# Kernel tuning notes

Hardware: AMD Instinct MI355X
Metric: run time of the kernel (lower is better)

Reference implementation:

```python
import jax, jax.numpy as jnp
import numpy as np

N = 256
DIAM = 2.0 * np.pi
VISC = 1e-3
DRAG = 0.1
SCALE = 1.0
PEAK_K = 4
DT = 0.001            # stable_time_step: min(0.001, 0.5*dx/max_velocity) = 0.001 here
NUM_STEPS = 90        # int(T/0.001), T=0.09
RECORD_EVERY = 30
BATCH = 8

# Carpenter-Kennedy low-storage RK4 / Crank-Nicolson tableau (jax-cfd crank_nicolson_rk4)
ALPHAS = (0.0, 0.1496590219993, 0.3704009573644, 0.6222557631345, 0.9582821306748, 1.0)
BETAS = (0.0, -0.4178904745, -1.192151694643, -1.697784692471, -1.514183444257)
GAMMAS = (0.1496590219993, 0.3792103129999, 0.8229550293869, 0.6994504559488, 0.1530572479681)


def _consts():
    kx = jnp.fft.fftfreq(N, d=DIAM / N).astype(jnp.float32)      # cycles / unit length
    ky = jnp.fft.rfftfreq(N, d=DIAM / N).astype(jnp.float32)
    KX, KY = jnp.meshgrid(kx, ky, indexing='ij')                 # [N, N//2+1]
    lap = -(2.0 * np.pi) ** 2 * (KX ** 2 + KY ** 2)              # (2*pi*i*k)^2, real
    lap_nz = lap.at[0, 0].set(1.0)
    # 2/3-rule brick wall dealiasing filter
    third = N // 3
    filt = jnp.zeros((N, N // 2 + 1), jnp.float32)
    filt = filt.at[:third, :third + 1].set(1.0)
    filt = filt.at[-third:, :third + 1].set(1.0)
    # Kolmogorov forcing u=(scale*sin(k y), 0) -> vorticity forcing -scale*k*cos(k y)
    y = (jnp.arange(N, dtype=jnp.float32) + 0.5) * (DIAM / N)    # cell centers
    f = -SCALE * PEAK_K * jnp.cos(PEAK_K * y)[None, :] * jnp.ones((N, 1), jnp.float32)
    f_hat = jnp.fft.rfft2(f)                                     # [N, N//2+1] complex
    return KX, KY, lap, lap_nz, filt, f_hat


def setup_inputs() -> dict:
    key = jax.random.key(0)
    w = jax.random.normal(key, (BATCH, N, N), jnp.float32)
    # band-pass around peak wavenumber to mimic a smooth initial vorticity field
    kx = jnp.fft.fftfreq(N, d=1.0 / N)
    ky = jnp.fft.rfftfreq(N, d=1.0 / N)
    kk = jnp.sqrt(kx[:, None] ** 2 + ky[None, :] ** 2)
    amp = jnp.exp(-0.5 * ((kk - PEAK_K) / 2.0) ** 2).astype(jnp.float32)
    w = jnp.fft.irfft2(jnp.fft.rfft2(w) * amp, s=(N, N))
    w = 5.0 * w / jnp.max(jnp.abs(w))
    return {"vort_init": w.astype(jnp.float32)}


def reference(vort_init) -> jnp.ndarray:
    KX, KY, lap, lap_nz, filt, f_hat = _consts()
    lin = VISC * lap - DRAG                 # implicit (linear) operator symbol, real
    two_pi_i = 2j * jnp.pi

    def explicit(w_hat):
        # vorticity -> velocity via streamfunction
        psi_hat = -w_hat / lap_nz
        vx = jnp.fft.irfft2(two_pi_i * KY * psi_hat, s=(N, N))
        vy = jnp.fft.irfft2(-two_pi_i * KX * psi_hat, s=(N, N))
        gx = jnp.fft.irfft2(two_pi_i * KX * w_hat, s=(N, N))
        gy = jnp.fft.irfft2(two_pi_i * KY * w_hat, s=(N, N))
        adv_hat = jnp.fft.rfft2(-(vx * gx + vy * gy)) * filt   # dealiased advection
        return adv_hat + f_hat

    @jax.checkpoint
    def step(w_hat):
        u = w_hat
        h = jnp.zeros_like(w_hat)
        for k in range(5):
            h = explicit(u) + BETAS[k] * h
            mu = 0.5 * DT * (ALPHAS[k + 1] - ALPHAS[k])
            u = (u + GAMMAS[k] * DT * h + mu * lin * u) / (1.0 - mu * lin)
        return u

    def body(u, _):
        u = step(u)
        return u, u

    w0 = jnp.fft.rfft2(vort_init)                    # [B, N, N//2+1]
    _, traj = jax.lax.scan(body, w0, None, length=NUM_STEPS)
    rec = traj[RECORD_EVERY - 1::RECORD_EVERY]       # [3, B, N, N//2+1]
    return jnp.fft.irfft2(rec, s=(N, N))             # [3, B, N, N]
```

## Files before the change

### kernel.cpp

```cpp
#include <hip/hip_runtime.h>
#include <math.h>

#define PI_F 3.14159265358979323846f
typedef unsigned long long u64;

__constant__ float c_beta[5] = {0.0f, -0.4178904745f, -1.192151694643f,
                                -1.697784692471f, -1.514183444257f};
__constant__ float c_gdt[5]  = {1.496590219993e-4f, 3.792103129999e-4f,
                                8.229550293869e-4f, 6.994504559488e-4f,
                                1.530572479681e-4f};
__constant__ float c_mu[5]   = {7.482951099965e-5f, 1.1037096768255e-4f,
                                1.2592740288505e-4f, 1.6801318377015e-4f,
                                2.08589346626e-5f};

struct __align__(128) Line { int v; int pad[31]; };

struct SharedMem {
  float sAr[2048], sAi[2048], sBr[2048], sBi[2048];
  float twr[128], twi[128];
  float t0r[430], t0i[430], t1r[430], t1i[430];
  float t2r[430], t2i[430], t3r[430], t3i[430];
};

__device__ __forceinline__ int swz(int i) { return i ^ (i >> 3); }

__device__ __forceinline__ float2 ldc(const float2* p)
{
  u64 v = __hip_atomic_load((const u64*)p, __ATOMIC_RELAXED, __HIP_MEMORY_SCOPE_AGENT);
  float2 f; __builtin_memcpy(&f, &v, 8); return f;
}
__device__ __forceinline__ void stg(float2* p, float2 f) { *p = f; }

__device__ __forceinline__ void bar_all(Line* arr, int n, int idx, int gen)
{
  __syncthreads();
  if (threadIdx.x == 0)
    __hip_atomic_store(&arr[idx].v, gen, __ATOMIC_RELAXED, __HIP_MEMORY_SCOPE_AGENT);
  if (threadIdx.x < 64) {
    bool done = false;
    while (!done) {
      bool ok = true;
      for (int w = threadIdx.x; w < n; w += 64)
        if (__hip_atomic_load(&arr[w].v, __ATOMIC_RELAXED, __HIP_MEMORY_SCOPE_AGENT) < gen)
          ok = false;
      done = __all(ok);
      if (!done) __builtin_amdgcn_s_sleep(2);
    }
    __builtin_amdgcn_sched_barrier(0);
  }
  __syncthreads();
}

__device__ __forceinline__ void bar_sync(Line* arr, Line* rel, int n, int idx,
                                         bool lead, int gen, bool fenced)
{
  const int t = threadIdx.x;
  __syncthreads();
  if (t == 0) {
    __builtin_amdgcn_s_waitcnt(0);
    __builtin_amdgcn_sched_barrier(0);
    if (fenced)
      __hip_atomic_store(&arr[idx].v, gen, __ATOMIC_RELEASE, __HIP_MEMORY_SCOPE_AGENT);
    else
      __hip_atomic_store(&arr[idx].v, gen, __ATOMIC_RELAXED, __HIP_MEMORY_SCOPE_AGENT);
  }
  if (lead && t < 64) {
    bool done = false;
    while (!done) {
      bool ok = true;
      for (int w = t; w < n; w += 64)
        if (__hip_atomic_load(&arr[w].v, __ATOMIC_RELAXED, __HIP_MEMORY_SCOPE_AGENT) < gen)
          ok = false;
      done = __all(ok);
      if (!done) __builtin_amdgcn_s_sleep(1);
    }
    __builtin_amdgcn_sched_barrier(0);
    if (fenced)
      (void)__hip_atomic_load(&arr[t & 7].v, __ATOMIC_ACQUIRE, __HIP_MEMORY_SCOPE_AGENT);
    if (t < 8) {
      if (fenced)
        __hip_atomic_store(&rel[t].v, gen, __ATOMIC_RELEASE, __HIP_MEMORY_SCOPE_AGENT);
      else
        __hip_atomic_store(&rel[t].v, gen, __ATOMIC_RELAXED, __HIP_MEMORY_SCOPE_AGENT);
    }
  }
  if (t == 0) {
    Line* f = &rel[idx & 7];
    while (__hip_atomic_load(&f->v, __ATOMIC_RELAXED, __HIP_MEMORY_SCOPE_AGENT) < gen)
      __builtin_amdgcn_s_sleep(1);
    if (fenced)
      (void)__hip_atomic_load(&f->v, __ATOMIC_ACQUIRE, __HIP_MEMORY_SCOPE_AGENT);
    __builtin_amdgcn_sched_barrier(0);
  }
  __syncthreads();
}

template<int B, bool INVERSE>
__device__ __forceinline__ void fftB(SharedMem& sh, int t)
{
  float *sr = sh.sAr, *si = sh.sAi, *dr = sh.sBr, *di = sh.sBi;
#pragma unroll
  for (int s = 0; s < 8; s += 2) {
    __syncthreads();
    const int m  = 1 << s;
    const int k  = t & (m - 1);
    const int e  = (t >> s) & 1;
    const int p  = (t >> (s + 1)) & 1;
    const int q0 = (t >> (s + 2)) << s;
    const int i0 = q0 + k;
    const float w1r = sh.twr[q0];
    const float w1i = INVERSE ? -sh.twi[q0] : sh.twi[q0];
    const float w2r = sh.twr[q0 << 1];
    const float w2i = INVERSE ? -sh.twi[q0 << 1] : sh.twi[q0 << 1];
#pragma unroll
    for (int f = 0; f < B; ++f) {
      const int base = f * 256;
      float S0r = sr[base + i0],       S0i = si[base + i0];
      float S1r = sr[base + i0 + 128], S1i = si[base + i0 + 128];
      float S2r = sr[base + i0 + 64],  S2i = si[base + i0 + 64];
      float S3r = sr[base + i0 + 192], S3i = si[base + i0 + 192];
      float Ar, Ai, Br, Bi;
      if (e == 0) { Ar = S0r + S1r; Ai = S0i + S1i; Br = S2r + S3r; Bi = S2i + S3i; }
      else {
        float xr = S0r - S1r, xi = S0i - S1i;
        Ar = xr * w1r - xi * w1i; Ai = xr * w1i + xi * w1r;
        float yr = S2r - S3r, yi = S2i - S3i;
        float tr = yr * w1r - yi * w1i, ti = yr * w1i + yi * w1r;
        Br = INVERSE ? -ti : ti; Bi = INVERSE ? tr : -tr;
      }
      float Or, Oi;
      if (p == 0) { Or = Ar + Br; Oi = Ai + Bi; }
      else {
        float xr = Ar - Br, xi = Ai - Bi;
        Or = xr * w2r - xi * w2i; Oi = xr * w2i + xi * w2r;
      }
      dr[base + t] = Or; di[base + t] = Oi;
    }
    float* tp;
    tp = sr; sr = dr; dr = tp;
    tp = si; si = di; di = tp;
  }
  __syncthreads();
}

template<bool INVERSE>
__device__ __forceinline__ void bfly4(const float (&vr)[4], const float (&vi)[4],
    float w1r, float w1i, float w2r, float w2i,
    float (&o_r)[4], float (&o_i)[4])
{
  float Ar  = vr[0] + vr[2], Ai  = vi[0] + vi[2];
  float dr_ = vr[0] - vr[2], di_ = vi[0] - vi[2];
  float Atr = dr_ * w1r - di_ * w1i, Ati = dr_ * w1i + di_ * w1r;
  float Br  = vr[1] + vr[3], Bi  = vi[1] + vi[3];
  float er_ = vr[1] - vr[3], ei_ = vi[1] - vi[3];
  float tr_ = er_ * w1r - ei_ * w1i, ti_ = er_ * w1i + ei_ * w1r;
  float Btr = INVERSE ? -ti_ : ti_;
  float Bti = INVERSE ?  tr_ : -tr_;
  o_r[0] = Ar + Br;   o_i[0] = Ai + Bi;
  o_r[1] = Atr + Btr; o_i[1] = Ati + Bti;
  float c0r = Ar - Br,   c0i = Ai - Bi;
  float c1r = Atr - Btr, c1i = Ati - Bti;
  o_r[2] = c0r * w2r - c0i * w2i; o_i[2] = c0r * w2i + c0i * w2r;
  o_r[3] = c1r * w2r - c1i * w2i; o_i[3] = c1r * w2i + c1i * w2r;
}

template<int B, bool INVERSE>
__device__ __forceinline__ void fft_reg(SharedMem& sh, int t,
                                        float (&vr)[4], float (&vi)[4])
{
  const int f  = t >> 6;
  const int tt = t & 63;
  const bool act = (f < B);
  __syncthreads();
#pragma unroll
  for (int s4 = 0; s4 < 4; ++s4) {
    const int s = s4 * 2;
    float o_r[4], o_i[4];
    int pos0 = 0;
    if (act) {
      const int k  = tt & ((1 << s) - 1);
      const int q0 = tt - k;
      const float w1r = sh.twr[q0];
      const float w1i = INVERSE ? -sh.twi[q0] : sh.twi[q0];
      const float w2r = sh.twr[q0 << 1];
      const float w2i = INVERSE ? -sh.twi[q0 << 1] : sh.twi[q0 << 1];
      bfly4<INVERSE>(vr, vi, w1r, w1i, w2r, w2i, o_r, o_i);
      pos0 = ((tt >> s) << (s + 2)) + k;
    }
    if (s4 < 3) {
      float* xr = (s4 & 1) ? sh.sBr : sh.sAr;
      float* xi = (s4 & 1) ? sh.sBi : sh.sAi;
      if (act) {
#pragma unroll
        for (int m = 0; m < 4; ++m) {
          const int w_ = f * 256 + swz(pos0 + (m << s));
          xr[w_] = o_r[m]; xi[w_] = o_i[m];
        }
      }
      __syncthreads();
      if (act) {
#pragma unroll
        for (int j = 0; j < 4; ++j) {
          const int rd = f * 256 + swz(tt + 64 * j);
          vr[j] = xr[rd]; vi[j] = xi[rd];
        }
      }
    } else if (act) {
#pragma unroll
      for (int j = 0; j < 4; ++j) { vr[j] = o_r[j]; vi[j] = o_i[j]; }
    }
  }
}

template<bool INVERSE>
__device__ __forceinline__ void fft_reg_dual(SharedMem& sh, int t,
    float (&ar)[4], float (&ai)[4], float (&br)[4], float (&bi)[4])
{
  const int f  = t >> 6;
  const int tt = t & 63;
  __syncthreads();
#pragma unroll
  for (int s4 = 0; s4 < 4; ++s4) {
    const int s = s4 * 2;
    const int k  = tt & ((1 << s) - 1);
    const int q0 = tt - k;
    const float w1r = sh.twr[q0];
    const float w1i = INVERSE ? -sh.twi[q0] : sh.twi[q0];
    const float w2r = sh.twr[q0 << 1];
    const float w2i = INVERSE ? -sh.twi[q0 << 1] : sh.twi[q0 << 1];
    float oAr[4], oAi[4], oBr[4], oBi[4];
    bfly4<INVERSE>(ar, ai, w1r, w1i, w2r, w2i, oAr, oAi);
    bfly4<INVERSE>(br, bi, w1r, w1i, w2r, w2i, oBr, oBi);
    if (s4 < 3) {
      const int pos0 = ((tt >> s) << (s + 2)) + k;
      float* xr = (s4 & 1) ? sh.sBr : sh.sAr;
      float* xi = (s4 & 1) ? sh.sBi : sh.sAi;
      const int baseA = f * 256, baseB = (f + 4) * 256;
#pragma unroll
      for (int m = 0; m < 4; ++m) {
        const int w_ = swz(pos0 + (m << s));
        xr[baseA + w_] = oAr[m]; xi[baseA + w_] = oAi[m];
        xr[baseB + w_] = oBr[m]; xi[baseB + w_] = oBi[m];
      }
      __syncthreads();
#pragma unroll
      for (int j = 0; j < 4; ++j) {
        const int rd = swz(tt + 64 * j);
        ar[j] = xr[baseA + rd]; ai[j] = xi[baseA + rd];
        br[j] = xr[baseB + rd]; bi[j] = xi[baseB + rd];
      }
    } else {
#pragma unroll
      for (int j = 0; j < 4; ++j) {
        ar[j] = oAr[j]; ai[j] = oAi[j];
        br[j] = oBr[j]; bi[j] = oBi[j];
      }
    }
  }
}


__device__ __forceinline__ void build_Z2(const float* t0r_, const float* t0i_,
    const float* t1r_, const float* t1i_, int f, int tt,
    float (&zr)[4], float (&zi)[4])
{
#pragma unroll
  for (int j = 0; j < 4; ++j) {
    int n = tt + 64 * j;
    bool low = (n <= 128);
    int kk = low ? n : 256 - n;
    float ar = 0.f, ai = 0.f, br = 0.f, bi = 0.f;
    if (kk <= 85) {
      ar = t0r_[kk * 5 + f]; ai = t0i_[kk * 5 + f];
      br = t1r_[kk * 5 + f]; bi = t1i_[kk * 5 + f];
    }
    zr[j] = low ? (ar - bi) : (ar + bi);
    zi[j] = low ? (ai + br) : (br - ai);
  }
}

__device__ __forceinline__ void real_item4_reg(SharedMem& sh, int t, int b, int x0,
    const float2* __restrict__ G, float2* __restrict__ NL1)
{
  const int f = t >> 6, tt = t & 63;
  __syncthreads();
  for (int i = t; i < 344; i += 256) {
    int ky = i >> 2, xl = i & 3;
    float2 a0 = ldc(&G[(((size_t)0 * 8 + b) * 129 + ky) * 256 + x0 + xl]);
    float2 a1 = ldc(&G[(((size_t)1 * 8 + b) * 129 + ky) * 256 + x0 + xl]);
    float2 a2 = ldc(&G[(((size_t)2 * 8 + b) * 129 + ky) * 256 + x0 + xl]);
    float2 a3 = ldc(&G[(((size_t)3 * 8 + b) * 129 + ky) * 256 + x0 + xl]);
    sh.t0r[ky * 5 + xl] = a0.x; sh.t0i[ky * 5 + xl] = a0.y;
    sh.t1r[ky * 5 + xl] = a1.x; sh.t1i[ky * 5 + xl] = a1.y;
    sh.t2r[ky * 5 + xl] = a2.x; sh.t2i[ky * 5 + xl] = a2.y;
    sh.t3r[ky * 5 + xl] = a3.x; sh.t3i[ky * 5 + xl] = a3.y;
  }
  __syncthreads();
  float ar_[4], ai_[4], br_[4], bi_[4];
  build_Z2(sh.t0r, sh.t0i, sh.t1r, sh.t1i, f, tt, ar_, ai_);
  build_Z2(sh.t2r, sh.t2i, sh.t3r, sh.t3i, f, tt, br_, bi_);
  fft_reg_dual<true>(sh, t, ar_, ai_, br_, bi_);
  float nl[4];
#pragma unroll
  for (int j = 0; j < 4; ++j)
    nl[j] = -(ar_[j] * br_[j] + ai_[j] * bi_[j]);
  __syncthreads();
#pragma unroll
  for (int j = 0; j < 4; ++j) sh.sAr[f * 256 + tt + 64 * j] = nl[j];
  __syncthreads();
  float wr2[4], wi2[4];
  if (f < 2) {
#pragma unroll
    for (int j = 0; j < 4; ++j) {
      wr2[j] = sh.sAr[(2 * f) * 256 + tt + 64 * j];
      wi2[j] = sh.sAr[(2 * f + 1) * 256 + tt + 64 * j];
    }
  }
  fft_reg<2, false>(sh, t, wr2, wi2);
  if (f < 2) {
#pragma unroll
    for (int j = 0; j < 4; ++j) {
      sh.sBr[f * 256 + tt + 64 * j] = wr2[j];
      sh.sBi[f * 256 + tt + 64 * j] = wi2[j];
    }
  }
  __syncthreads();
  if (t <= 85) {
    int mI = (256 - t) & 255;
#pragma unroll
    for (int p = 0; p < 2; ++p) {
      float zr_ = sh.sBr[p * 256 + t],  zi_ = sh.sBi[p * 256 + t];
      float wr_ = sh.sBr[p * 256 + mI], wi_ = sh.sBi[p * 256 + mI];
      stg(&NL1[((size_t)b * 86 + t) * 256 + x0 + 2 * p],
          make_float2(0.5f * (zr_ + wr_), 0.5f * (zi_ - wi_)));
      stg(&NL1[((size_t)b * 86 + t) * 256 + x0 + 2 * p + 1],
          make_float2(0.5f * (zi_ + wi_), 0.5f * (wr_ - zr_)));
    }
  }
}

__device__ __forceinline__ void spectral_item2_reg(SharedMem& sh, int t, int b, int ky0,
    const float2* __restrict__ NL1, float2* __restrict__ u, float2* __restrict__ h,
    float2* __restrict__ G, float2* __restrict__ rec,
    float beta, float gdt, float mu, bool doUpdate, int recIdx)
{
  const int f = t >> 6, tt = t & 63;
  const size_t r0 = ((size_t)b * 129 + ky0) * 256;

  if (doUpdate) {
    float ar[4], ai[4];
    if (f < 2) {
#pragma unroll
      for (int j = 0; j < 4; ++j) {
        float2 nv = ldc(&NL1[((size_t)b * 86 + ky0 + f) * 256 + tt + 64 * j]);
        ar[j] = nv.x; ai[j] = nv.y;
      }
    }
    fft_reg<2, false>(sh, t, ar, ai);
    if (f < 2) {
      const int ky = ky0 + f;
      const size_t row = r0 + (size_t)f * 256;
#pragma unroll
      for (int j = 0; j < 4; ++j) {
        const int kx = tt + 64 * j;
        const bool keep = (kx < 85) || (kx >= 171);
        float advr = keep ? ar[j] : 0.f;
        float advi = keep ? ai[j] : 0.f;
        if (kx == 0 && ky == 4) {
          float s_, c_;
          __sincosf(PI_F / 64.0f, &s_, &c_);
          advr -= 131072.0f * c_;
          advi -= 131072.0f * s_;
        }
        float hr = advr, hi = advi;
        if (beta != 0.0f) {
          float2 hh = h[row + kx];
          hr += beta * hh.x; hi += beta * hh.y;
        }
        const int jx = (kx < 128) ? kx : kx - 256;
        const float k2   = (float)(jx * jx + ky * ky);
        const float lin  = -0.001f * k2 - 0.1f;
        const float anum = 1.0f + mu * lin;
        const float invd = 1.0f / (1.0f - mu * lin);
        float2 uu = u[row + kx];
        float urv = (uu.x * anum + gdt * hr) * invd;
        float uiv = (uu.y * anum + gdt * hi) * invd;
        u[row + kx] = make_float2(urv, uiv);
        h[row + kx] = make_float2(hr, hi);
        if (recIdx >= 0)
          stg(&rec[((size_t)recIdx * 8 + b) * (129 * 256) + (size_t)ky * 256 + kx],
              make_float2(urv, uiv));
      }
    }
    __syncthreads();
  }

  float u0r[4], u0i[4], u1r[4], u1i[4];
#pragma unroll
  for (int j = 0; j < 4; ++j) {
    float2 a = u[r0 + tt + 64 * j];
    float2 c = u[r0 + 256 + tt + 64 * j];
    u0r[j] = a.x; u0i[j] = a.y; u1r[j] = c.x; u1i[j] = c.y;
  }

  const float NRM = 1.0f / 65536.0f;
  const float fy0 = (float)ky0, fy1 = (float)(ky0 + 1);
  float x0r[4], x0i[4], x1r[4], x1i[4];
#pragma unroll
  for (int j = 0; j < 4; ++j) {
    const int kx = tt + 64 * j;
    const int jx = (kx < 128) ? kx : kx - 256;
    const float fjx = (float)jx;
    {
      const float k2 = (float)(jx * jx + ky0 * ky0);
      const float il = (k2 == 0.f) ? 1.f : (-1.f / k2);
      const float urN = u0r[j] * NRM, uiN = u0i[j] * NRM;
      const float psr = -urN * il, psi_ = -uiN * il;
      if      (f == 0) { x0r[j] = -fy0 * psi_; x0i[j] =  fy0 * psr; }
      else if (f == 1) { x0r[j] =  fjx * psi_; x0i[j] = -fjx * psr; }
      else if (f == 2) { x0r[j] = -fjx * uiN;  x0i[j] =  fjx * urN; }
      else             { x0r[j] = -fy0 * uiN;  x0i[j] =  fy0 * urN; }
    }
    {
      const int ky1 = ky0 + 1;
      const float k2 = (float)(jx * jx + ky1 * ky1);
      const float il = (k2 == 0.f) ? 1.f : (-1.f / k2);
      const float urN = u1r[j] * NRM, uiN = u1i[j] * NRM;
      const float psr = -urN * il, psi_ = -uiN * il;
      if      (f == 0) { x1r[j] = -fy1 * psi_; x1i[j] =  fy1 * psr; }
      else if (f == 1) { x1r[j] =  fjx * psi_; x1i[j] = -fjx * psr; }
      else if (f == 2) { x1r[j] = -fjx * uiN;  x1i[j] =  fjx * urN; }
      else             { x1r[j] = -fy1 * uiN;  x1i[j] =  fy1 * urN; }
    }
  }
  fft_reg_dual<true>(sh, t, x0r, x0i, x1r, x1i);
#pragma unroll
  for (int j = 0; j < 4; ++j) {
    stg(&G[(((size_t)f * 8 + b) * 129 + ky0) * 256 + tt + 64 * j],
        make_float2(x0r[j], x0i[j]));
    stg(&G[(((size_t)f * 8 + b) * 129 + ky0 + 1) * 256 + tt + 64 * j],
        make_float2(x1r[j], x1i[j]));
  }
}

__global__ __launch_bounds__(256, 2) void k_persist(
    const float* __restrict__ vort, float* __restrict__ out,
    float2* __restrict__ u, float2* __restrict__ h,
    float2* __restrict__ G, float2* __restrict__ NL1, float2* __restrict__ rec,
    Line* __restrict__ bar)
{
  const int t   = threadIdx.x;
  const int blk = blockIdx.x;
  const int NBg = gridDim.x;

  Line* arrGrid = bar;
  Line* relGrid = bar + 1024;
  Line* arrGrpA = bar + 1032;
  Line* relGrpA = bar + 1032 + 2048;
  Line* regL    = bar + 1032 + 2048 + 64;

  __shared__ SharedMem sh;
  __shared__ int s_x, s_wi;

  if (t < 128) {
    float s_, c_;
    __sincosf(-(2.0f * PI_F / 256.0f) * (float)t, &s_, &c_);
    sh.twr[t] = c_; sh.twi[t] = s_;
  }

  if (t == 0) {
    int x;
    asm volatile("s_getreg_b32 %0, hwreg(HW_REG_XCC_ID)" : "=s"(x));
    x &= 15;
    s_x  = x;
    s_wi = atomicAdd(&regL[x].v, 1);
  }
  __syncthreads();

  int gen = 0;
  bar_sync(arrGrid, relGrid, NBg, blk, blk == 0, ++gen, true);

  int tot = 0, mn = 1 << 30, mx = 0;
  for (int i = 0; i < 8; ++i) {
    int c = regL[i].v;
    tot += c; mn = min(mn, c); mx = max(mx, c);
  }
  const bool fast = (tot == NBg) && (mn > 0) && (mx <= 256);
  int g, wi, nW;
  if (fast) { g = s_x;     wi = s_wi;     nW = regL[g].v; }
  else      { g = blk & 7; wi = blk >> 3; nW = NBg >> 3;  }
  Line* arr = arrGrpA + g * 256;
  Line* rel = relGrpA + g * 8;
  const bool lead = (wi == 0);

#define GBAR() do { ++gen; if (fast) bar_all(arr, nW, wi, gen); \
                    else bar_sync(arr, rel, nW, wi, lead, gen, true); } while (0)

  float2* W1 = rec + (size_t)g * (129 * 256);
  for (int w = wi; w < 64; w += nW) {
    const int x0 = w * 4;
#pragma unroll
    for (int p = 0; p < 2; ++p) {
      sh.sAr[p * 256 + t] = vort[((size_t)g * 256 + x0 + 2 * p) * 256 + t];
      sh.sAi[p * 256 + t] = vort[((size_t)g * 256 + x0 + 2 * p + 1) * 256 + t];
    }
    fftB<2, false>(sh, t);
    if (t < 129) {
      int mI = (256 - t) & 255;
#pragma unroll
      for (int p = 0; p < 2; ++p) {
        float zr = sh.sAr[p * 256 + t],  zi = sh.sAi[p * 256 + t];
        float wr = sh.sAr[p * 256 + mI], wi2 = sh.sAi[p * 256 + mI];
        stg(&W1[(size_t)t * 256 + x0 + 2 * p],
            make_float2(0.5f * (zr + wr), 0.5f * (zi - wi2)));
        stg(&W1[(size_t)t * 256 + x0 + 2 * p + 1],
            make_float2(0.5f * (zi + wi2), 0.5f * (wr - zr)));
      }
    }
    __syncthreads();
  }
  GBAR();

  for (int w = wi; w < 43; w += nW) {
    const int ky0 = w * 2;
#pragma unroll
    for (int f = 0; f < 2; ++f) {
      float2 v = ldc(&W1[(size_t)(ky0 + f) * 256 + t]);
      sh.sAr[f * 256 + t] = v.x; sh.sAi[f * 256 + t] = v.y;
    }
    fftB<2, false>(sh, t);
#pragma unroll
    for (int f = 0; f < 2; ++f)
      u[((size_t)g * 129 + ky0 + f) * 256 + t] =
        make_float2(sh.sAr[f * 256 + t], sh.sAi[f * 256 + t]);
  }
  for (int w = wi; w < 43; w += nW)
    spectral_item2_reg(sh, t, g, w * 2, NL1, u, h, G, rec, 0.f, 0.f, 0.f, false, -1);

  for (int step = 1; step <= 90; ++step) {
    for (int k = 0; k < 5; ++k) {
      GBAR();
      for (int w = wi; w < 64; w += nW)
        real_item4_reg(sh, t, g, w * 4, G, NL1);
      GBAR();
      const int recIdx = (k == 4 && step % 30 == 0) ? (step / 30 - 1) : -1;
      for (int w = wi; w < 43; w += nW)
        spectral_item2_reg(sh, t, g, w * 2, NL1, u, h, G, rec,
                           c_beta[k], c_gdt[k], c_mu[k], true, recIdx);
    }
  }
  GBAR();

  for (int w = wi; w < 129; w += nW) {
#pragma unroll
    for (int j = 0; j < 2; ++j) {
      int idx = w * 2 + j, r = idx / 86, ky = idx % 86;
      float2 v = ldc(&rec[(((size_t)r * 8 + g) * 129 + ky) * 256 + t]);
      sh.sAr[j * 256 + t] = v.x; sh.sAi[j * 256 + t] = v.y;
    }
    fftB<2, true>(sh, t);
#pragma unroll
    for (int j = 0; j < 2; ++j) {
      int idx = w * 2 + j, r = idx / 86, ky = idx % 86;
      stg(&G[(((size_t)r * 8 + g) * 129 + ky) * 256 + t],
          make_float2(sh.sAr[j * 256 + t], sh.sAi[j * 256 + t]));
    }
  }
  GBAR();

  const float NRM = 1.0f / 65536.0f;
  for (int w = wi; w < 192; w += nW) {
    const int r = w / 64, xh = w % 64, x0 = xh * 4;
    __syncthreads();
    for (int i = t; i < 344; i += 256) {
      int ky = i >> 2, xl = i & 3;
      float2 a = ldc(&G[(((size_t)r * 8 + g) * 129 + ky) * 256 + x0 + xl]);
      sh.t0r[ky * 5 + xl] = a.x; sh.t0i[ky * 5 + xl] = a.y;
    }
    __syncthreads();
    const bool lower = (t <= 128);
    const int  kk    = lower ? t : 256 - t;
#pragma unroll
    for (int f = 0; f < 2; ++f) {
      float ar = 0.f, ai = 0.f, br = 0.f, bi = 0.f;
      if (kk <= 85) {
        ar = sh.t0r[kk * 5 + 2 * f];     ai = sh.t0i[kk * 5 + 2 * f];
        br = sh.t0r[kk * 5 + 2 * f + 1]; bi = sh.t0i[kk * 5 + 2 * f + 1];
      }
      sh.sAr[f * 256 + t] = lower ? (ar - bi) : (ar + bi);
      sh.sAi[f * 256 + t] = lower ? (ai + br) : (br - ai);
    }
    fftB<2, true>(sh, t);
#pragma unroll
    for (int f = 0; f < 2; ++f) {
      out[((((size_t)r * 8 + g) * 256) + x0 + 2 * f) * 256 + t]     = sh.sAr[f * 256 + t] * NRM;
      out[((((size_t)r * 8 + g) * 256) + x0 + 2 * f + 1) * 256 + t] = sh.sAi[f * 256 + t] * NRM;
    }
    __syncthreads();
  }
#undef GBAR
}

extern "C" void kernel_launch(void* const* d_in, const int* in_sizes, int n_in,
                              void* d_out, int out_size, void* d_ws, size_t ws_size,
                              hipStream_t stream)
{
  const float* vort = (const float*)d_in[0];
  float* out = (float*)d_out;

  float2* base = (float2*)d_ws;
  float2* u    = base;
  float2* h    = u + 264192;
  float2* G    = h + 264192;
  float2* NL1  = G + 1056768;
  float2* rec  = NL1 + 176128;
  Line*   bar  = (Line*)(rec + 792576);
  const int nLines = 1024 + 8 + 2048 + 64 + 16;

  hipMemsetAsync(bar, 0, (size_t)nLines * sizeof(Line), stream);

  int maxPerCU = 0;
  hipOccupancyMaxActiveBlocksPerMultiprocessor(&maxPerCU, k_persist, 256, 0);
  int NBg = maxPerCU * 256;
  if (NBg <= 0)  NBg = 512;
  if (NBg > 512) NBg = 512;
  NBg &= ~63;
  if (NBg < 64)  NBg = 64;

  void* args[] = {(void*)&vort, (void*)&out, (void*)&u, (void*)&h,
                  (void*)&G, (void*)&NL1, (void*)&rec, (void*)&bar};
  hipError_t e = hipLaunchCooperativeKernel(k_persist, dim3(NBg), dim3(256),
                                            args, 0, stream);
  if (e != hipSuccess) {
    hipLaunchKernelGGL(k_persist, dim3(NBg), dim3(256), 0, stream,
                       vort, out, u, h, G, NL1, rec, bar);
  }
}
```

Baseline: 7.701 ms.

## Make per-line FFT stages wave-synchronous and use a stage-dependent LDS swizzle

```diff
diff --git a/kernel.cpp b/kernel.cpp
--- a/kernel.cpp
+++ b/kernel.cpp
@@ -22,7 +22,10 @@
   float t2r[430], t2i[430], t3r[430], t3i[430];
 };
 
-__device__ __forceinline__ int swz(int i) { return i ^ (i >> 3); }
+__device__ __forceinline__ int swz(int i, int s4)
+{
+  return (i & ~31) | ((i + ((i >> 5) << s4)) & 31);
+}
 
 __device__ __forceinline__ float2 ldc(const float2* p)
 {
@@ -164,48 +167,40 @@
   o_r[3] = c1r * w2r - c1i * w2i; o_i[3] = c1r * w2i + c1i * w2r;
 }
 
-template<int B, bool INVERSE>
+template<int B, bool INVERSE, int RO>
 __device__ __forceinline__ void fft_reg(SharedMem& sh, int t,
                                         float (&vr)[4], float (&vi)[4])
 {
   const int f  = t >> 6;
   const int tt = t & 63;
-  const bool act = (f < B);
-  __syncthreads();
+  if (f >= B) return;
+  const int base = (f + RO) * 256;
 #pragma unroll
   for (int s4 = 0; s4 < 4; ++s4) {
     const int s = s4 * 2;
+    const int k  = tt & ((1 << s) - 1);
+    const int q0 = tt - k;
+    const float w1r = sh.twr[q0];
+    const float w1i = INVERSE ? -sh.twi[q0] : sh.twi[q0];
+    const float w2r = sh.twr[q0 << 1];
+    const float w2i = INVERSE ? -sh.twi[q0 << 1] : sh.twi[q0 << 1];
     float o_r[4], o_i[4];
-    int pos0 = 0;
-    if (act) {
-      const int k  = tt & ((1 << s) - 1);
-      const int q0 = tt - k;
-      const float w1r = sh.twr[q0];
-      const float w1i = INVERSE ? -sh.twi[q0] : sh.twi[q0];
-      const float w2r = sh.twr[q0 << 1];
-      const float w2i = INVERSE ? -sh.twi[q0 << 1] : sh.twi[q0 << 1];
-      bfly4<INVERSE>(vr, vi, w1r, w1i, w2r, w2i, o_r, o_i);
-      pos0 = ((tt >> s) << (s + 2)) + k;
-    }
+    bfly4<INVERSE>(vr, vi, w1r, w1i, w2r, w2i, o_r, o_i);
     if (s4 < 3) {
+      const int pos0 = ((tt >> s) << (s + 2)) + k;
       float* xr = (s4 & 1) ? sh.sBr : sh.sAr;
       float* xi = (s4 & 1) ? sh.sBi : sh.sAi;
-      if (act) {
-#pragma unroll
-        for (int m = 0; m < 4; ++m) {
-          const int w_ = f * 256 + swz(pos0 + (m << s));
-          xr[w_] = o_r[m]; xi[w_] = o_i[m];
-        }
-      }
-      __syncthreads();
-      if (act) {
-#pragma unroll
-        for (int j = 0; j < 4; ++j) {
-          const int rd = f * 256 + swz(tt + 64 * j);
-          vr[j] = xr[rd]; vi[j] = xi[rd];
-        }
-      }
-    } else if (act) {
+#pragma unroll
+      for (int m = 0; m < 4; ++m) {
+        const int w_ = base + swz(pos0 + (m << s), s4);
+        xr[w_] = o_r[m]; xi[w_] = o_i[m];
+      }
+#pragma unroll
+      for (int j = 0; j < 4; ++j) {
+        const int rd = base + swz(tt + 64 * j, s4);
+        vr[j] = xr[rd]; vi[j] = xi[rd];
+      }
+    } else {
 #pragma unroll
       for (int j = 0; j < 4; ++j) { vr[j] = o_r[j]; vi[j] = o_i[j]; }
     }
@@ -218,7 +213,7 @@
 {
   const int f  = t >> 6;
   const int tt = t & 63;
-  __syncthreads();
+  const int baseA = f * 256, baseB = (f + 4) * 256;
 #pragma unroll
   for (int s4 = 0; s4 < 4; ++s4) {
     const int s = s4 * 2;
@@ -235,17 +230,15 @@
       const int pos0 = ((tt >> s) << (s + 2)) + k;
       float* xr = (s4 & 1) ? sh.sBr : sh.sAr;
       float* xi = (s4 & 1) ? sh.sBi : sh.sAi;
-      const int baseA = f * 256, baseB = (f + 4) * 256;
 #pragma unroll
       for (int m = 0; m < 4; ++m) {
-        const int w_ = swz(pos0 + (m << s));
+        const int w_ = swz(pos0 + (m << s), s4);
         xr[baseA + w_] = oAr[m]; xi[baseA + w_] = oAi[m];
         xr[baseB + w_] = oBr[m]; xi[baseB + w_] = oBi[m];
       }
-      __syncthreads();
 #pragma unroll
       for (int j = 0; j < 4; ++j) {
-        const int rd = swz(tt + 64 * j);
+        const int rd = swz(tt + 64 * j, s4);
         ar[j] = xr[baseA + rd]; ai[j] = xi[baseA + rd];
         br[j] = xr[baseB + rd]; bi[j] = xi[baseB + rd];
       }
@@ -283,7 +276,6 @@
     const float2* __restrict__ G, float2* __restrict__ NL1)
 {
   const int f = t >> 6, tt = t & 63;
-  __syncthreads();
   for (int i = t; i < 344; i += 256) {
     int ky = i >> 2, xl = i & 3;
     float2 a0 = ldc(&G[(((size_t)0 * 8 + b) * 129 + ky) * 256 + x0 + xl]);
@@ -304,7 +296,6 @@
 #pragma unroll
   for (int j = 0; j < 4; ++j)
     nl[j] = -(ar_[j] * br_[j] + ai_[j] * bi_[j]);
-  __syncthreads();
 #pragma unroll
   for (int j = 0; j < 4; ++j) sh.sAr[f * 256 + tt + 64 * j] = nl[j];
   __syncthreads();
@@ -316,7 +307,7 @@
       wi2[j] = sh.sAr[(2 * f + 1) * 256 + tt + 64 * j];
     }
   }
-  fft_reg<2, false>(sh, t, wr2, wi2);
+  fft_reg<2, false, 4>(sh, t, wr2, wi2);
   if (f < 2) {
 #pragma unroll
     for (int j = 0; j < 4; ++j) {
@@ -356,7 +347,7 @@
         ar[j] = nv.x; ai[j] = nv.y;
       }
     }
-    fft_reg<2, false>(sh, t, ar, ai);
+    fft_reg<2, false, 0>(sh, t, ar, ai);
     if (f < 2) {
       const int ky = ky0 + f;
       const size_t row = r0 + (size_t)f * 256;
@@ -534,6 +525,7 @@
       u[((size_t)g * 129 + ky0 + f) * 256 + t] =
         make_float2(sh.sAr[f * 256 + t], sh.sAi[f * 256 + t]);
   }
+  __syncthreads();
   for (int w = wi; w < 43; w += nW)
     spectral_item2_reg(sh, t, g, w * 2, NL1, u, h, G, rec, 0.f, 0.f, 0.f, false, -1);
 
@@ -565,6 +557,7 @@
       stg(&G[(((size_t)r * 8 + g) * 129 + ky) * 256 + t],
           make_float2(sh.sAr[j * 256 + t], sh.sAi[j * 256 + t]));
     }
+    __syncthreads();
   }
   GBAR();
 
```

New measurement: 6.759 ms. 1.14x faster.
